# Optimization experiments

Hardware: AMD Instinct MI355X
Metric: run time of the kernel (lower is better)

The kernel has to match this reference:

```python
import jax, jax.numpy as jnp
import numpy as np
import math

B, S, E, H = 2, 2048, 2048, 16
HD = E // H // 2  # 64, per-head dim of each differential half
DEPTH = 12
LAMBDA_INIT = 0.8 - 0.6 * math.exp(-0.3 * DEPTH)
EPS = 1e-5


def setup_inputs() -> dict:
    key = jax.random.key(0)
    ks = jax.random.split(key, 10)
    sc = 0.02
    return {
        "x": jax.random.normal(ks[0], (B, S, E), jnp.float32),
        "Wq": jax.random.normal(ks[1], (E, E), jnp.float32) * sc,
        "Wk": jax.random.normal(ks[2], (E, E), jnp.float32) * sc,
        "Wv": jax.random.normal(ks[3], (E, E), jnp.float32) * sc,
        "Wo": jax.random.normal(ks[4], (E, E), jnp.float32) * sc,
        "lambda_q1": jax.random.normal(ks[5], (HD,), jnp.float32) * 0.1,
        "lambda_k1": jax.random.normal(ks[6], (HD,), jnp.float32) * 0.1,
        "lambda_q2": jax.random.normal(ks[7], (HD,), jnp.float32) * 0.1,
        "lambda_k2": jax.random.normal(ks[8], (HD,), jnp.float32) * 0.1,
        "gamma": jnp.ones((2 * HD,), jnp.float32),
    }


def _rope_interleaved(x, cos, sin):
    # x: [b, s, h, d]; cos/sin: [s, d//2]; pairs are (0,1),(2,3),...
    xe, xo = x[..., 0::2], x[..., 1::2]
    c = cos[None, :, None, :]
    s = sin[None, :, None, :]
    oe = xe * c - xo * s
    oo = xe * s + xo * c
    return jnp.stack([oe, oo], axis=-1).reshape(x.shape)


def reference(x, Wq, Wk, Wv, Wo, lambda_q1, lambda_k1, lambda_q2, lambda_k2, gamma):
    b, t, _ = x.shape
    # rotary tables (rotary dim == HD, interleaved)
    angle = 1.0 / 10000 ** jnp.linspace(0.0, 1.0, HD // 2, dtype=jnp.float32)
    freqs = jnp.arange(t, dtype=jnp.float32)[:, None] * angle  # [t, HD//2]
    cos, sin = jnp.cos(freqs), jnp.sin(freqs)

    q = (x @ Wq.T).reshape(b, t, 2 * H, HD)
    k = (x @ Wk.T).reshape(b, t, 2 * H, HD)
    v = (x @ Wv.T).reshape(b, t, H, 2 * HD)  # concat(v1, v2) along last dim

    q = _rope_interleaved(q, cos, sin)
    k = _rope_interleaved(k, cos, sin)

    q = q.reshape(b, t, H, 2, HD)
    k = k.reshape(b, t, H, 2, HD)
    q1, q2 = q[:, :, :, 0], q[:, :, :, 1]
    k1, k2 = k[:, :, :, 0], k[:, :, :, 1]

    scale = HD ** -0.5  # flash_attn default softmax scale
    # branch 1: softmax(q1 k1) @ [v1|v2]
    s1 = jnp.einsum("bthd,bshd->bhts", q1, k1) * scale
    p1 = jax.nn.softmax(s1, axis=-1)
    o1 = jnp.einsum("bhts,bshd->bthd", p1, v)  # [b,t,H,2*HD]
    # branch 2: softmax(q2 k2) @ [v1|v2]
    s2 = jnp.einsum("bthd,bshd->bhts", q2, k2) * scale
    p2 = jax.nn.softmax(s2, axis=-1)
    o2 = jnp.einsum("bhts,bshd->bthd", p2, v)

    lam1 = jnp.exp(jnp.sum(lambda_q1 * lambda_k1))
    lam2 = jnp.exp(jnp.sum(lambda_q2 * lambda_k2))
    lam = lam1 - lam2 + LAMBDA_INIT

    attn = o1 - lam * o2  # [b,t,H,2*HD]
    # RMSNorm over last dim (2*HD) with affine gamma
    rms = jax.lax.rsqrt(jnp.mean(attn * attn, axis=-1, keepdims=True) + EPS)
    attn = attn * rms * gamma
    attn = attn * (1.0 - LAMBDA_INIT)
    attn = attn.reshape(b, t, H * 2 * HD)
    return attn @ Wo.T
```

## Files before the change

kernel.cpp:

```cpp
#include <hip/hip_runtime.h>
#include <cstdint>
#include <cstddef>

typedef unsigned short u16;
typedef __attribute__((ext_vector_type(8))) short short8;
typedef __attribute__((ext_vector_type(4))) float f32x4;

#define MFMA_B16(a,b,c) __builtin_amdgcn_mfma_f32_16x16x32_bf16((a),(b),(c),0,0,0)

#define S_LEN 2048
#define EMB 2048
#define QKV_N 6144
#define HD 64
#define LAMBDA_INIT_F 0.78360576653162f
#define ONE_MINUS_LI 0.21639423346838f

static __device__ __forceinline__ u16 f2bf(float f) {
  unsigned u = __float_as_uint(f);
  unsigned r = ((u >> 16) & 1u) + 0x7fffu;
  return (u16)((u + r) >> 16);
}
static __device__ __forceinline__ float bf2f(u16 h) {
  return __uint_as_float(((unsigned)h) << 16);
}
static __device__ __forceinline__ unsigned cvt_pk_bf16(float lo, float hi) {
  unsigned r;
  asm("v_cvt_pk_bf16_f32 %0, %1, %2" : "=v"(r) : "v"(lo), "v"(hi));
  return r;
}
static __device__ __forceinline__ void gload_lds16(const u16* g, u16* l) {
  __builtin_amdgcn_global_load_lds((const __attribute__((address_space(1))) void*)g,
                                   (__attribute__((address_space(3))) void*)l, 16, 0, 0);
}

__global__ void cvt_f32_bf16(const float* __restrict__ s, u16* __restrict__ d, int n4) {
  int i = blockIdx.x * 256 + threadIdx.x;
  if (i >= n4) return;
  f32x4 v = *(const f32x4*)&s[i * 4];
  unsigned lo = cvt_pk_bf16(v[0], v[1]);
  unsigned hi = cvt_pk_bf16(v[2], v[3]);
  *(unsigned long long*)&d[i * 4] = (unsigned long long)lo | ((unsigned long long)hi << 32);
}

template <int BF16OUT>
__global__ __launch_bounds__(256, 2) void gemm_bt(const u16* __restrict__ A,
                                                  const u16* __restrict__ B,
                                                  void* __restrict__ Cout,
                                                  int M, int N, int K) {
  __shared__ u16 As[128 * 32];
  __shared__ u16 Bs[128 * 32];
  const int tid = threadIdx.x;
  const int lane = tid & 63, wv = tid >> 6;
  const int bm = blockIdx.x * 128, bn = blockIdx.y * 128;
  const int wr = (wv >> 1) * 64, wc = (wv & 1) * 64;
  const int lr = lane & 15, hk = lane >> 4;

  const int r0 = tid >> 2;
  const int c0 = (tid & 3) * 8;
  const u16* ga = A + (size_t)(bm + r0) * K + c0;
  const u16* gb = B + (size_t)(bn + r0) * K + c0;
  const size_t rstep = (size_t)64 * K;

  f32x4 acc[4][4] = {};

  for (int k0 = 0; k0 < K; k0 += 32) {
    __syncthreads();
    gload_lds16(ga + k0,         &As[(tid) * 8]);
    gload_lds16(ga + rstep + k0, &As[(tid + 256) * 8]);
    gload_lds16(gb + k0,         &Bs[(tid) * 8]);
    gload_lds16(gb + rstep + k0, &Bs[(tid + 256) * 8]);
    __syncthreads();
    short8 af[4], bfv[4];
#pragma unroll
    for (int i = 0; i < 4; i++) af[i] = *(const short8*)&As[(wr + i * 16 + lr) * 32 + hk * 8];
#pragma unroll
    for (int j = 0; j < 4; j++) bfv[j] = *(const short8*)&Bs[(wc + j * 16 + lr) * 32 + hk * 8];
#pragma unroll
    for (int i = 0; i < 4; i++)
#pragma unroll
      for (int j = 0; j < 4; j++)
        acc[i][j] = MFMA_B16(af[i], bfv[j], acc[i][j]);
  }

  if (BF16OUT) {
    u16* C = (u16*)Cout;
#pragma unroll
    for (int i = 0; i < 4; i++)
#pragma unroll
      for (int j = 0; j < 4; j++)
#pragma unroll
        for (int r = 0; r < 4; r++) {
          int row = bm + wr + i * 16 + hk * 4 + r;
          int col = bn + wc + j * 16 + lr;
          C[(size_t)row * N + col] = f2bf(acc[i][j][r]);
        }
  } else {
    float* C = (float*)Cout;
#pragma unroll
    for (int i = 0; i < 4; i++)
#pragma unroll
      for (int j = 0; j < 4; j++)
#pragma unroll
        for (int r = 0; r < 4; r++) {
          int row = bm + wr + i * 16 + hk * 4 + r;
          int col = bn + wc + j * 16 + lr;
          C[(size_t)row * N + col] = acc[i][j][r];
        }
  }
}

__global__ void rope_kernel(u16* __restrict__ qkv) {
  int idx = blockIdx.x * 256 + threadIdx.x;
  int p = idx & 31;
  int u = (idx >> 5) & 63;
  int m = idx >> 11;
  int t = m & (S_LEN - 1);
  int col = (u < 32) ? (u * 64 + 2 * p) : (EMB + (u - 32) * 64 + 2 * p);
  u16* ptr = qkv + (size_t)m * QKV_N + col;
  unsigned v = *(unsigned*)ptr;
  float xe = bf2f((u16)(v & 0xffff));
  float xo = bf2f((u16)(v >> 16));
  float w = expf((float)p * (-9.210340371976184f / 31.0f));
  float ang = (float)t * w;
  float sn, cs;
  sincosf(ang, &sn, &cs);
  float oe = xe * cs - xo * sn;
  float oo = xe * sn + xo * cs;
  *(unsigned*)ptr = (unsigned)f2bf(oe) | (((unsigned)f2bf(oo)) << 16);
}

#define SW(row, colByte) ((((row)) << 7) + ((colByte) ^ (((row) & 7) << 4)))

__global__ __launch_bounds__(256, 2) void attn_kernel(
    const u16* __restrict__ qkv, u16* __restrict__ attnb,
    const float* __restrict__ lq1, const float* __restrict__ lk1,
    const float* __restrict__ lq2, const float* __restrict__ lk2,
    const float* __restrict__ gamma) {
  __shared__ u16 K1s[64 * 64];
  __shared__ u16 K2s[64 * 64];
  __shared__ u16 VTs[128 * 64];
  __shared__ u16 Ps[4 * 2 * 16 * 64];

  const int g = blockIdx.x;
  const int xcd = g & 7;
  const int gi = g >> 3;
  const int bh = xcd * 4 + (gi >> 5);
  const int qt = gi & 31;
  const int b = bh >> 4, h = bh & 15;

  const int tid = threadIdx.x, lane = tid & 63, wv = tid >> 6;
  const int lr = lane & 15, hk = lane >> 4;

  float d1 = lq1[lane] * lk1[lane];
  float d2 = lq2[lane] * lk2[lane];
#pragma unroll
  for (int off = 32; off; off >>= 1) { d1 += __shfl_xor(d1, off); d2 += __shfl_xor(d2, off); }
  const float lam = __expf(d1) - __expf(d2) + LAMBDA_INIT_F;

  const int qrow = qt * 64 + wv * 16 + lr;
  const u16* qp = qkv + (size_t)(b * S_LEN + qrow) * QKV_N;
  short8 q1f[2], q2f[2];
  q1f[0] = *(const short8*)&qp[(2 * h) * 64 + hk * 8];
  q1f[1] = *(const short8*)&qp[(2 * h) * 64 + 32 + hk * 8];
  q2f[0] = *(const short8*)&qp[(2 * h + 1) * 64 + hk * 8];
  q2f[1] = *(const short8*)&qp[(2 * h + 1) * 64 + 32 + hk * 8];

  f32x4 o1a[8] = {};
  f32x4 o2a[8] = {};
  float l1p = 0.f, l2p = 0.f;

  const int gl_row = wv * 8 + (lane >> 3);
  const int gl_cb  = ((lane & 7) ^ (lane >> 3)) * 8;
  u16* k1d = &K1s[(wv * 8) * 64 + lane * 8];
  u16* k2d = &K2s[(wv * 8) * 64 + lane * 8];

  const int vkv = (tid & 31) * 2;
  const int vd0 = (tid >> 5) * 8;

  const u16* kb1 = qkv + (size_t)b * S_LEN * QKV_N + EMB + (2 * h) * 64;
  const u16* kb2 = kb1 + 64;
  const u16* vbp = qkv + (size_t)b * S_LEN * QKV_N + 2 * EMB + h * 128;

  char* P1 = (char*)&Ps[(wv * 2 + 0) * 16 * 64];
  char* P2 = (char*)&Ps[(wv * 2 + 1) * 16 * 64];
  char* VTc = (char*)VTs;

  for (int kv0 = 0; kv0 < S_LEN; kv0 += 64) {
    __syncthreads();
    {
      const u16* g1 = kb1 + (size_t)(kv0 + gl_row) * QKV_N + gl_cb;
      const u16* g2 = kb2 + (size_t)(kv0 + gl_row) * QKV_N + gl_cb;
      gload_lds16(g1, k1d);
      gload_lds16(g1 + (size_t)32 * QKV_N, k1d + 32 * 64);
      gload_lds16(g2, k2d);
      gload_lds16(g2 + (size_t)32 * QKV_N, k2d + 32 * 64);
    }
    {
      const u16* vs = vbp + (size_t)(kv0 + vkv) * QKV_N + vd0;
      short8 a0 = *(const short8*)vs;
      short8 a1 = *(const short8*)(vs + QKV_N);
      short8 b0 = *(const short8*)(vs + 64);
      short8 b1 = *(const short8*)(vs + QKV_N + 64);
#pragma unroll
      for (int j = 0; j < 8; j++) {
        unsigned pk0 = (unsigned)(u16)a0[j] | (((unsigned)(u16)a1[j]) << 16);
        *(unsigned*)(VTc + SW(vd0 + j, vkv * 2)) = pk0;
        unsigned pk1 = (unsigned)(u16)b0[j] | (((unsigned)(u16)b1[j]) << 16);
        *(unsigned*)(VTc + SW(vd0 + 64 + j, vkv * 2)) = pk1;
      }
    }
    __syncthreads();

#pragma unroll
    for (int st = 0; st < 2; st++) {
      const char* Ks = st ? (char*)K2s : (char*)K1s;
      const short8* qf = st ? q2f : q1f;
      char* Pw = st ? P2 : P1;
      float lacc = 0.f;
#pragma unroll
      for (int kt = 0; kt < 4; kt++) {
        f32x4 s = {0.f, 0.f, 0.f, 0.f};
        int row = kt * 16 + lr;
        short8 ka0 = *(const short8*)(Ks + SW(row, hk * 16));
        short8 ka1 = *(const short8*)(Ks + SW(row, 64 + hk * 16));
        s = MFMA_B16(ka0, qf[0], s);
        s = MFMA_B16(ka1, qf[1], s);
        float e0 = __expf(s[0] * 0.125f);
        float e1 = __expf(s[1] * 0.125f);
        float e2 = __expf(s[2] * 0.125f);
        float e3 = __expf(s[3] * 0.125f);
        lacc += (e0 + e1) + (e2 + e3);
        unsigned plo = cvt_pk_bf16(e0, e1);
        unsigned phi = cvt_pk_bf16(e2, e3);
        *(unsigned long long*)(Pw + SW(lr, kt * 32 + hk * 8)) =
            (unsigned long long)plo | ((unsigned long long)phi << 32);
      }
      if (st) l2p += lacc; else l1p += lacc;
    }
    asm volatile("" ::: "memory");

    short8 p10 = *(const short8*)(P1 + SW(lr, hk * 16));
    short8 p11 = *(const short8*)(P1 + SW(lr, 64 + hk * 16));
    short8 p20 = *(const short8*)(P2 + SW(lr, hk * 16));
    short8 p21 = *(const short8*)(P2 + SW(lr, 64 + hk * 16));
#pragma unroll
    for (int dt = 0; dt < 8; dt++) {
      int row = dt * 16 + lr;
      short8 va0 = *(const short8*)(VTc + SW(row, hk * 16));
      short8 va1 = *(const short8*)(VTc + SW(row, 64 + hk * 16));
      o1a[dt] = MFMA_B16(va0, p10, o1a[dt]);
      o1a[dt] = MFMA_B16(va1, p11, o1a[dt]);
      o2a[dt] = MFMA_B16(va0, p20, o2a[dt]);
      o2a[dt] = MFMA_B16(va1, p21, o2a[dt]);
    }
  }

  float l1 = l1p; l1 += __shfl_xor(l1, 16); l1 += __shfl_xor(l1, 32);
  float l2 = l2p; l2 += __shfl_xor(l2, 16); l2 += __shfl_xor(l2, 32);
  const float inv1 = 1.f / l1;
  const float inv2 = 1.f / l2;

  float av[8][4];
  float ss = 0.f;
#pragma unroll
  for (int dt = 0; dt < 8; dt++)
#pragma unroll
    for (int r = 0; r < 4; r++) {
      float a = o1a[dt][r] * inv1 - lam * (o2a[dt][r] * inv2);
      av[dt][r] = a;
      ss += a * a;
    }
  ss += __shfl_xor(ss, 16); ss += __shfl_xor(ss, 32);
  const float sc2 = rsqrtf(ss * (1.f / 128.f) + 1e-5f) * ONE_MINUS_LI;

  u16* orow = attnb + (size_t)(b * S_LEN + qrow) * EMB + h * 128;
#pragma unroll
  for (int dt = 0; dt < 8; dt++) {
    int d = dt * 16 + hk * 4;
    f32x4 gv = *(const f32x4*)&gamma[d];
    unsigned plo = cvt_pk_bf16(av[dt][0] * gv[0] * sc2, av[dt][1] * gv[1] * sc2);
    unsigned phi = cvt_pk_bf16(av[dt][2] * gv[2] * sc2, av[dt][3] * gv[3] * sc2);
    *(unsigned long long*)&orow[d] = (unsigned long long)plo | ((unsigned long long)phi << 32);
  }
}

extern "C" void kernel_launch(void* const* d_in, const int* in_sizes, int n_in,
                              void* d_out, int out_size, void* d_ws, size_t ws_size,
                              hipStream_t stream) {
  (void)in_sizes; (void)n_in; (void)out_size; (void)ws_size;
  const float* x   = (const float*)d_in[0];
  const float* Wq  = (const float*)d_in[1];
  const float* Wk  = (const float*)d_in[2];
  const float* Wv  = (const float*)d_in[3];
  const float* Wo  = (const float*)d_in[4];
  const float* lq1 = (const float*)d_in[5];
  const float* lk1 = (const float*)d_in[6];
  const float* lq2 = (const float*)d_in[7];
  const float* lk2 = (const float*)d_in[8];
  const float* gam = (const float*)d_in[9];

  char* ws = (char*)d_ws;
  u16* xb    = (u16*)(ws);
  u16* Wcat  = (u16*)(ws + 16777216);
  u16* Wob   = (u16*)(ws + 41943040);
  u16* qkv   = (u16*)(ws + 50331648);
  u16* attnb = xb;

  const int NE = EMB * EMB;
  cvt_f32_bf16<<<(2 * NE / 4 + 255) / 256, 256, 0, stream>>>(x, xb, 2 * NE / 4);
  cvt_f32_bf16<<<(NE / 4 + 255) / 256, 256, 0, stream>>>(Wq, Wcat, NE / 4);
  cvt_f32_bf16<<<(NE / 4 + 255) / 256, 256, 0, stream>>>(Wk, Wcat + NE, NE / 4);
  cvt_f32_bf16<<<(NE / 4 + 255) / 256, 256, 0, stream>>>(Wv, Wcat + 2 * NE, NE / 4);
  cvt_f32_bf16<<<(NE / 4 + 255) / 256, 256, 0, stream>>>(Wo, Wob, NE / 4);

  dim3 g1(4096 / 128, QKV_N / 128);
  gemm_bt<1><<<g1, 256, 0, stream>>>(xb, Wcat, qkv, 4096, QKV_N, EMB);

  rope_kernel<<<(4096 * 64 * 32) / 256, 256, 0, stream>>>(qkv);

  attn_kernel<<<1024, 256, 0, stream>>>(qkv, attnb, lq1, lk1, lq2, lk2, gam);

  dim3 g2(4096 / 128, EMB / 128);
  gemm_bt<0><<<g2, 256, 0, stream>>>(attnb, Wob, d_out, 4096, EMB, EMB);
}
```

Measured before the change: 360.9 us.

## Process two 16-row query tiles per wave to reuse K/V LDS loads

```diff
diff --git a/kernel.cpp b/kernel.cpp
--- a/kernel.cpp
+++ b/kernel.cpp
@@ -14,6 +14,7 @@
 #define HD 64
 #define LAMBDA_INIT_F 0.78360576653162f
 #define ONE_MINUS_LI 0.21639423346838f
+#define EXP2_SCALE 0.18033688011112042f
 
 static __device__ __forceinline__ u16 f2bf(float f) {
   unsigned u = __float_as_uint(f);
@@ -139,13 +140,13 @@
   __shared__ u16 K1s[64 * 64];
   __shared__ u16 K2s[64 * 64];
   __shared__ u16 VTs[128 * 64];
-  __shared__ u16 Ps[4 * 2 * 16 * 64];
+  __shared__ u16 Ps[4 * 4 * 16 * 64];
 
   const int g = blockIdx.x;
   const int xcd = g & 7;
   const int gi = g >> 3;
-  const int bh = xcd * 4 + (gi >> 5);
-  const int qt = gi & 31;
+  const int bh = xcd * 4 + (gi >> 4);
+  const int qt = gi & 15;
   const int b = bh >> 4, h = bh & 15;
 
   const int tid = threadIdx.x, lane = tid & 63, wv = tid >> 6;
@@ -157,17 +158,21 @@
   for (int off = 32; off; off >>= 1) { d1 += __shfl_xor(d1, off); d2 += __shfl_xor(d2, off); }
   const float lam = __expf(d1) - __expf(d2) + LAMBDA_INIT_F;
 
-  const int qrow = qt * 64 + wv * 16 + lr;
-  const u16* qp = qkv + (size_t)(b * S_LEN + qrow) * QKV_N;
-  short8 q1f[2], q2f[2];
-  q1f[0] = *(const short8*)&qp[(2 * h) * 64 + hk * 8];
-  q1f[1] = *(const short8*)&qp[(2 * h) * 64 + 32 + hk * 8];
-  q2f[0] = *(const short8*)&qp[(2 * h + 1) * 64 + hk * 8];
-  q2f[1] = *(const short8*)&qp[(2 * h + 1) * 64 + 32 + hk * 8];
-
-  f32x4 o1a[8] = {};
-  f32x4 o2a[8] = {};
-  float l1p = 0.f, l2p = 0.f;
+  const int qrowA = qt * 128 + wv * 32 + lr;
+  const int qrowB = qrowA + 16;
+  const u16* qpA = qkv + (size_t)(b * S_LEN + qrowA) * QKV_N;
+  const u16* qpB = qkv + (size_t)(b * S_LEN + qrowB) * QKV_N;
+  short8 q1fA0 = *(const short8*)&qpA[(2 * h) * 64 + hk * 8];
+  short8 q1fA1 = *(const short8*)&qpA[(2 * h) * 64 + 32 + hk * 8];
+  short8 q2fA0 = *(const short8*)&qpA[(2 * h + 1) * 64 + hk * 8];
+  short8 q2fA1 = *(const short8*)&qpA[(2 * h + 1) * 64 + 32 + hk * 8];
+  short8 q1fB0 = *(const short8*)&qpB[(2 * h) * 64 + hk * 8];
+  short8 q1fB1 = *(const short8*)&qpB[(2 * h) * 64 + 32 + hk * 8];
+  short8 q2fB0 = *(const short8*)&qpB[(2 * h + 1) * 64 + hk * 8];
+  short8 q2fB1 = *(const short8*)&qpB[(2 * h + 1) * 64 + 32 + hk * 8];
+
+  f32x4 o1A[8] = {}, o1B[8] = {}, o2A[8] = {}, o2B[8] = {};
+  float l1pA = 0.f, l1pB = 0.f, l2pA = 0.f, l2pB = 0.f;
 
   const int gl_row = wv * 8 + (lane >> 3);
   const int gl_cb  = ((lane & 7) ^ (lane >> 3)) * 8;
@@ -181,8 +186,10 @@
   const u16* kb2 = kb1 + 64;
   const u16* vbp = qkv + (size_t)b * S_LEN * QKV_N + 2 * EMB + h * 128;
 
-  char* P1 = (char*)&Ps[(wv * 2 + 0) * 16 * 64];
-  char* P2 = (char*)&Ps[(wv * 2 + 1) * 16 * 64];
+  char* P1A = (char*)&Ps[(wv * 4 + 0) * 16 * 64];
+  char* P1B = (char*)&Ps[(wv * 4 + 1) * 16 * 64];
+  char* P2A = (char*)&Ps[(wv * 4 + 2) * 16 * 64];
+  char* P2B = (char*)&Ps[(wv * 4 + 3) * 16 * 64];
   char* VTc = (char*)VTs;
 
   for (int kv0 = 0; kv0 < S_LEN; kv0 += 64) {
@@ -214,73 +221,121 @@
 #pragma unroll
     for (int st = 0; st < 2; st++) {
       const char* Ks = st ? (char*)K2s : (char*)K1s;
-      const short8* qf = st ? q2f : q1f;
-      char* Pw = st ? P2 : P1;
-      float lacc = 0.f;
+      const short8 qa0 = st ? q2fA0 : q1fA0;
+      const short8 qa1 = st ? q2fA1 : q1fA1;
+      const short8 qb0 = st ? q2fB0 : q1fB0;
+      const short8 qb1 = st ? q2fB1 : q1fB1;
+      char* PwA = st ? P2A : P1A;
+      char* PwB = st ? P2B : P1B;
+      float laccA = 0.f, laccB = 0.f;
 #pragma unroll
       for (int kt = 0; kt < 4; kt++) {
-        f32x4 s = {0.f, 0.f, 0.f, 0.f};
         int row = kt * 16 + lr;
         short8 ka0 = *(const short8*)(Ks + SW(row, hk * 16));
         short8 ka1 = *(const short8*)(Ks + SW(row, 64 + hk * 16));
-        s = MFMA_B16(ka0, qf[0], s);
-        s = MFMA_B16(ka1, qf[1], s);
-        float e0 = __expf(s[0] * 0.125f);
-        float e1 = __expf(s[1] * 0.125f);
-        float e2 = __expf(s[2] * 0.125f);
-        float e3 = __expf(s[3] * 0.125f);
-        lacc += (e0 + e1) + (e2 + e3);
-        unsigned plo = cvt_pk_bf16(e0, e1);
-        unsigned phi = cvt_pk_bf16(e2, e3);
-        *(unsigned long long*)(Pw + SW(lr, kt * 32 + hk * 8)) =
-            (unsigned long long)plo | ((unsigned long long)phi << 32);
+        f32x4 sA = {0.f, 0.f, 0.f, 0.f};
+        sA = MFMA_B16(ka0, qa0, sA);
+        sA = MFMA_B16(ka1, qa1, sA);
+        f32x4 sB = {0.f, 0.f, 0.f, 0.f};
+        sB = MFMA_B16(ka0, qb0, sB);
+        sB = MFMA_B16(ka1, qb1, sB);
+        float eA0 = __builtin_amdgcn_exp2f(sA[0] * EXP2_SCALE);
+        float eA1 = __builtin_amdgcn_exp2f(sA[1] * EXP2_SCALE);
+        float eA2 = __builtin_amdgcn_exp2f(sA[2] * EXP2_SCALE);
+        float eA3 = __builtin_amdgcn_exp2f(sA[3] * EXP2_SCALE);
+        laccA += (eA0 + eA1) + (eA2 + eA3);
+        unsigned pa0 = cvt_pk_bf16(eA0, eA1);
+        unsigned pa1 = cvt_pk_bf16(eA2, eA3);
+        *(unsigned long long*)(PwA + SW(lr, kt * 32 + hk * 8)) =
+            (unsigned long long)pa0 | ((unsigned long long)pa1 << 32);
+        float eB0 = __builtin_amdgcn_exp2f(sB[0] * EXP2_SCALE);
+        float eB1 = __builtin_amdgcn_exp2f(sB[1] * EXP2_SCALE);
+        float eB2 = __builtin_amdgcn_exp2f(sB[2] * EXP2_SCALE);
+        float eB3 = __builtin_amdgcn_exp2f(sB[3] * EXP2_SCALE);
+        laccB += (eB0 + eB1) + (eB2 + eB3);
+        unsigned pb0 = cvt_pk_bf16(eB0, eB1);
+        unsigned pb1 = cvt_pk_bf16(eB2, eB3);
+        *(unsigned long long*)(PwB + SW(lr, kt * 32 + hk * 8)) =
+            (unsigned long long)pb0 | ((unsigned long long)pb1 << 32);
       }
-      if (st) l2p += lacc; else l1p += lacc;
+      if (st) { l2pA += laccA; l2pB += laccB; }
+      else    { l1pA += laccA; l1pB += laccB; }
     }
     asm volatile("" ::: "memory");
 
-    short8 p10 = *(const short8*)(P1 + SW(lr, hk * 16));
-    short8 p11 = *(const short8*)(P1 + SW(lr, 64 + hk * 16));
-    short8 p20 = *(const short8*)(P2 + SW(lr, hk * 16));
-    short8 p21 = *(const short8*)(P2 + SW(lr, 64 + hk * 16));
+    short8 p10A = *(const short8*)(P1A + SW(lr, hk * 16));
+    short8 p11A = *(const short8*)(P1A + SW(lr, 64 + hk * 16));
+    short8 p10B = *(const short8*)(P1B + SW(lr, hk * 16));
+    short8 p11B = *(const short8*)(P1B + SW(lr, 64 + hk * 16));
+    short8 p20A = *(const short8*)(P2A + SW(lr, hk * 16));
+    short8 p21A = *(const short8*)(P2A + SW(lr, 64 + hk * 16));
+    short8 p20B = *(const short8*)(P2B + SW(lr, hk * 16));
+    short8 p21B = *(const short8*)(P2B + SW(lr, 64 + hk * 16));
 #pragma unroll
     for (int dt = 0; dt < 8; dt++) {
       int row = dt * 16 + lr;
       short8 va0 = *(const short8*)(VTc + SW(row, hk * 16));
       short8 va1 = *(const short8*)(VTc + SW(row, 64 + hk * 16));
-      o1a[dt] = MFMA_B16(va0, p10, o1a[dt]);
-      o1a[dt] = MFMA_B16(va1, p11, o1a[dt]);
-      o2a[dt] = MFMA_B16(va0, p20, o2a[dt]);
-      o2a[dt] = MFMA_B16(va1, p21, o2a[dt]);
-    }
-  }
-
-  float l1 = l1p; l1 += __shfl_xor(l1, 16); l1 += __shfl_xor(l1, 32);
-  float l2 = l2p; l2 += __shfl_xor(l2, 16); l2 += __shfl_xor(l2, 32);
-  const float inv1 = 1.f / l1;
-  const float inv2 = 1.f / l2;
-
-  float av[8][4];
-  float ss = 0.f;
-#pragma unroll
-  for (int dt = 0; dt < 8; dt++)
-#pragma unroll
-    for (int r = 0; r < 4; r++) {
-      float a = o1a[dt][r] * inv1 - lam * (o2a[dt][r] * inv2);
-      av[dt][r] = a;
-      ss += a * a;
-    }
-  ss += __shfl_xor(ss, 16); ss += __shfl_xor(ss, 32);
-  const float sc2 = rsqrtf(ss * (1.f / 128.f) + 1e-5f) * ONE_MINUS_LI;
-
-  u16* orow = attnb + (size_t)(b * S_LEN + qrow) * EMB + h * 128;
-#pragma unroll
-  for (int dt = 0; dt < 8; dt++) {
-    int d = dt * 16 + hk * 4;
-    f32x4 gv = *(const f32x4*)&gamma[d];
-    unsigned plo = cvt_pk_bf16(av[dt][0] * gv[0] * sc2, av[dt][1] * gv[1] * sc2);
-    unsigned phi = cvt_pk_bf16(av[dt][2] * gv[2] * sc2, av[dt][3] * gv[3] * sc2);
-    *(unsigned long long*)&orow[d] = (unsigned long long)plo | ((unsigned long long)phi << 32);
+      o1A[dt] = MFMA_B16(va0, p10A, o1A[dt]);
+      o1A[dt] = MFMA_B16(va1, p11A, o1A[dt]);
+      o1B[dt] = MFMA_B16(va0, p10B, o1B[dt]);
+      o1B[dt] = MFMA_B16(va1, p11B, o1B[dt]);
+      o2A[dt] = MFMA_B16(va0, p20A, o2A[dt]);
+      o2A[dt] = MFMA_B16(va1, p21A, o2A[dt]);
+      o2B[dt] = MFMA_B16(va0, p20B, o2B[dt]);
+      o2B[dt] = MFMA_B16(va1, p21B, o2B[dt]);
+    }
+  }
+
+  {
+    float l1 = l1pA; l1 += __shfl_xor(l1, 16); l1 += __shfl_xor(l1, 32);
+    float l2 = l2pA; l2 += __shfl_xor(l2, 16); l2 += __shfl_xor(l2, 32);
+    const float inv1 = 1.f / l1, inv2 = 1.f / l2;
+    float ss = 0.f;
+#pragma unroll
+    for (int dt = 0; dt < 8; dt++)
+#pragma unroll
+      for (int r = 0; r < 4; r++) {
+        float a = o1A[dt][r] * inv1 - lam * (o2A[dt][r] * inv2);
+        o1A[dt][r] = a;
+        ss += a * a;
+      }
+    ss += __shfl_xor(ss, 16); ss += __shfl_xor(ss, 32);
+    const float sc2 = rsqrtf(ss * (1.f / 128.f) + 1e-5f) * ONE_MINUS_LI;
+    u16* orow = attnb + (size_t)(b * S_LEN + qrowA) * EMB + h * 128;
+#pragma unroll
+    for (int dt = 0; dt < 8; dt++) {
+      int d = dt * 16 + hk * 4;
+      f32x4 gv = *(const f32x4*)&gamma[d];
+      unsigned plo = cvt_pk_bf16(o1A[dt][0] * gv[0] * sc2, o1A[dt][1] * gv[1] * sc2);
+      unsigned phi = cvt_pk_bf16(o1A[dt][2] * gv[2] * sc2, o1A[dt][3] * gv[3] * sc2);
+      *(unsigned long long*)&orow[d] = (unsigned long long)plo | ((unsigned long long)phi << 32);
+    }
+  }
+  {
+    float l1 = l1pB; l1 += __shfl_xor(l1, 16); l1 += __shfl_xor(l1, 32);
+    float l2 = l2pB; l2 += __shfl_xor(l2, 16); l2 += __shfl_xor(l2, 32);
+    const float inv1 = 1.f / l1, inv2 = 1.f / l2;
+    float ss = 0.f;
+#pragma unroll
+    for (int dt = 0; dt < 8; dt++)
+#pragma unroll
+      for (int r = 0; r < 4; r++) {
+        float a = o1B[dt][r] * inv1 - lam * (o2B[dt][r] * inv2);
+        o1B[dt][r] = a;
+        ss += a * a;
+      }
+    ss += __shfl_xor(ss, 16); ss += __shfl_xor(ss, 32);
+    const float sc2 = rsqrtf(ss * (1.f / 128.f) + 1e-5f) * ONE_MINUS_LI;
+    u16* orow = attnb + (size_t)(b * S_LEN + qrowB) * EMB + h * 128;
+#pragma unroll
+    for (int dt = 0; dt < 8; dt++) {
+      int d = dt * 16 + hk * 4;
+      f32x4 gv = *(const f32x4*)&gamma[d];
+      unsigned plo = cvt_pk_bf16(o1B[dt][0] * gv[0] * sc2, o1B[dt][1] * gv[1] * sc2);
+      unsigned phi = cvt_pk_bf16(o1B[dt][2] * gv[2] * sc2, o1B[dt][3] * gv[3] * sc2);
+      *(unsigned long long*)&orow[d] = (unsigned long long)plo | ((unsigned long long)phi << 32);
+    }
   }
 }
 
@@ -318,7 +373,7 @@
 
   rope_kernel<<<(4096 * 64 * 32) / 256, 256, 0, stream>>>(qkv);
 
-  attn_kernel<<<1024, 256, 0, stream>>>(qkv, attnb, lq1, lk1, lq2, lk2, gam);
+  attn_kernel<<<512, 256, 0, stream>>>(qkv, attnb, lq1, lk1, lq2, lk2, gam);
 
   dim3 g2(4096 / 128, EMB / 128);
   gemm_bt<0><<<g2, 256, 0, stream>>>(attnb, Wob, d_out, 4096, EMB, EMB);
```

After: 401.8 us. +11.3%, slower.

## Switch attention to 32x32x16 MFMA with 128-row query tiles per block

Applied to the files above, without the earlier changes.

```diff
diff --git a/kernel.cpp b/kernel.cpp
--- a/kernel.cpp
+++ b/kernel.cpp
@@ -5,8 +5,10 @@
 typedef unsigned short u16;
 typedef __attribute__((ext_vector_type(8))) short short8;
 typedef __attribute__((ext_vector_type(4))) float f32x4;
+typedef __attribute__((ext_vector_type(16))) float f32x16;
 
 #define MFMA_B16(a,b,c) __builtin_amdgcn_mfma_f32_16x16x32_bf16((a),(b),(c),0,0,0)
+#define MFMA32(a,b,c)  __builtin_amdgcn_mfma_f32_32x32x16_bf16((a),(b),(c),0,0,0)
 
 #define S_LEN 2048
 #define EMB 2048
@@ -14,6 +16,7 @@
 #define HD 64
 #define LAMBDA_INIT_F 0.78360576653162f
 #define ONE_MINUS_LI 0.21639423346838f
+#define EXP2_SCALE 0.18033688011112042f
 
 static __device__ __forceinline__ u16 f2bf(float f) {
   unsigned u = __float_as_uint(f);
@@ -131,6 +134,38 @@
 
 #define SW(row, colByte) ((((row)) << 7) + ((colByte) ^ (((row) & 7) << 4)))
 
+#define QKT(Kc, Q0, Q1, Q2, Q3, KT, Pc, LSUM)                                    \
+  do {                                                                           \
+    f32x16 s = {};                                                               \
+    s = MFMA32(*(const short8*)((Kc) + SW((KT) * 32 + l31, 0  + hi16)), Q0, s);  \
+    s = MFMA32(*(const short8*)((Kc) + SW((KT) * 32 + l31, 32 + hi16)), Q1, s);  \
+    s = MFMA32(*(const short8*)((Kc) + SW((KT) * 32 + l31, 64 + hi16)), Q2, s);  \
+    s = MFMA32(*(const short8*)((Kc) + SW((KT) * 32 + l31, 96 + hi16)), Q3, s);  \
+    _Pragma("unroll") for (int r = 0; r < 16; r += 4) {                          \
+      float e0 = __builtin_amdgcn_exp2f(s[r]     * EXP2_SCALE);                  \
+      float e1 = __builtin_amdgcn_exp2f(s[r + 1] * EXP2_SCALE);                  \
+      float e2 = __builtin_amdgcn_exp2f(s[r + 2] * EXP2_SCALE);                  \
+      float e3 = __builtin_amdgcn_exp2f(s[r + 3] * EXP2_SCALE);                  \
+      LSUM += (e0 + e1) + (e2 + e3);                                             \
+      unsigned lo_ = cvt_pk_bf16(e0, e1);                                        \
+      unsigned hi_ = cvt_pk_bf16(e2, e3);                                        \
+      *(unsigned long long*)((Pc) + SW(l31, (KT) * 64 + (r >> 2) * 16 + hi8)) =  \
+          (unsigned long long)lo_ | ((unsigned long long)hi_ << 32);             \
+    }                                                                            \
+  } while (0)
+
+#define PVD(DT, O1, O2)                                                          \
+  do {                                                                           \
+    short8 va0 = *(const short8*)(VTc + SW((DT) * 32 + l31, 0  + hi16));         \
+    short8 va1 = *(const short8*)(VTc + SW((DT) * 32 + l31, 32 + hi16));         \
+    short8 va2 = *(const short8*)(VTc + SW((DT) * 32 + l31, 64 + hi16));         \
+    short8 va3 = *(const short8*)(VTc + SW((DT) * 32 + l31, 96 + hi16));         \
+    O1 = MFMA32(va0, p1f0, O1); O1 = MFMA32(va1, p1f1, O1);                      \
+    O1 = MFMA32(va2, p1f2, O1); O1 = MFMA32(va3, p1f3, O1);                      \
+    O2 = MFMA32(va0, p2f0, O2); O2 = MFMA32(va1, p2f1, O2);                      \
+    O2 = MFMA32(va2, p2f2, O2); O2 = MFMA32(va3, p2f3, O2);                      \
+  } while (0)
+
 __global__ __launch_bounds__(256, 2) void attn_kernel(
     const u16* __restrict__ qkv, u16* __restrict__ attnb,
     const float* __restrict__ lq1, const float* __restrict__ lk1,
@@ -139,17 +174,20 @@
   __shared__ u16 K1s[64 * 64];
   __shared__ u16 K2s[64 * 64];
   __shared__ u16 VTs[128 * 64];
-  __shared__ u16 Ps[4 * 2 * 16 * 64];
+  __shared__ u16 Ps[4 * 2 * 32 * 64];
 
   const int g = blockIdx.x;
   const int xcd = g & 7;
   const int gi = g >> 3;
-  const int bh = xcd * 4 + (gi >> 5);
-  const int qt = gi & 31;
+  const int bh = xcd * 4 + (gi >> 4);
+  const int qt = gi & 15;
   const int b = bh >> 4, h = bh & 15;
 
   const int tid = threadIdx.x, lane = tid & 63, wv = tid >> 6;
-  const int lr = lane & 15, hk = lane >> 4;
+  const int l31 = lane & 31;
+  const int hi16 = (lane >> 5) * 16;
+  const int hi8 = (lane >> 5) * 8;
+  const int hi4 = (lane >> 5) * 4;
 
   float d1 = lq1[lane] * lk1[lane];
   float d2 = lq2[lane] * lk2[lane];
@@ -157,16 +195,20 @@
   for (int off = 32; off; off >>= 1) { d1 += __shfl_xor(d1, off); d2 += __shfl_xor(d2, off); }
   const float lam = __expf(d1) - __expf(d2) + LAMBDA_INIT_F;
 
-  const int qrow = qt * 64 + wv * 16 + lr;
-  const u16* qp = qkv + (size_t)(b * S_LEN + qrow) * QKV_N;
-  short8 q1f[2], q2f[2];
-  q1f[0] = *(const short8*)&qp[(2 * h) * 64 + hk * 8];
-  q1f[1] = *(const short8*)&qp[(2 * h) * 64 + 32 + hk * 8];
-  q2f[0] = *(const short8*)&qp[(2 * h + 1) * 64 + hk * 8];
-  q2f[1] = *(const short8*)&qp[(2 * h + 1) * 64 + 32 + hk * 8];
-
-  f32x4 o1a[8] = {};
-  f32x4 o2a[8] = {};
+  const int qbase = qt * 128 + wv * 32;
+  const u16* qp1 = qkv + (size_t)(b * S_LEN + qbase + l31) * QKV_N + (2 * h) * 64;
+  const u16* qp2 = qp1 + 64;
+  short8 q1f0 = *(const short8*)(qp1 + hi8);
+  short8 q1f1 = *(const short8*)(qp1 + 16 + hi8);
+  short8 q1f2 = *(const short8*)(qp1 + 32 + hi8);
+  short8 q1f3 = *(const short8*)(qp1 + 48 + hi8);
+  short8 q2f0 = *(const short8*)(qp2 + hi8);
+  short8 q2f1 = *(const short8*)(qp2 + 16 + hi8);
+  short8 q2f2 = *(const short8*)(qp2 + 32 + hi8);
+  short8 q2f3 = *(const short8*)(qp2 + 48 + hi8);
+
+  f32x16 o1t0 = {}, o1t1 = {}, o1t2 = {}, o1t3 = {};
+  f32x16 o2t0 = {}, o2t1 = {}, o2t2 = {}, o2t3 = {};
   float l1p = 0.f, l2p = 0.f;
 
   const int gl_row = wv * 8 + (lane >> 3);
@@ -181,9 +223,11 @@
   const u16* kb2 = kb1 + 64;
   const u16* vbp = qkv + (size_t)b * S_LEN * QKV_N + 2 * EMB + h * 128;
 
-  char* P1 = (char*)&Ps[(wv * 2 + 0) * 16 * 64];
-  char* P2 = (char*)&Ps[(wv * 2 + 1) * 16 * 64];
+  char* K1c = (char*)K1s;
+  char* K2c = (char*)K2s;
   char* VTc = (char*)VTs;
+  char* P1c = (char*)&Ps[(wv * 2 + 0) * 32 * 64];
+  char* P2c = (char*)&Ps[(wv * 2 + 1) * 32 * 64];
 
   for (int kv0 = 0; kv0 < S_LEN; kv0 += 64) {
     __syncthreads();
@@ -211,77 +255,56 @@
     }
     __syncthreads();
 
-#pragma unroll
-    for (int st = 0; st < 2; st++) {
-      const char* Ks = st ? (char*)K2s : (char*)K1s;
-      const short8* qf = st ? q2f : q1f;
-      char* Pw = st ? P2 : P1;
-      float lacc = 0.f;
-#pragma unroll
-      for (int kt = 0; kt < 4; kt++) {
-        f32x4 s = {0.f, 0.f, 0.f, 0.f};
-        int row = kt * 16 + lr;
-        short8 ka0 = *(const short8*)(Ks + SW(row, hk * 16));
-        short8 ka1 = *(const short8*)(Ks + SW(row, 64 + hk * 16));
-        s = MFMA_B16(ka0, qf[0], s);
-        s = MFMA_B16(ka1, qf[1], s);
-        float e0 = __expf(s[0] * 0.125f);
-        float e1 = __expf(s[1] * 0.125f);
-        float e2 = __expf(s[2] * 0.125f);
-        float e3 = __expf(s[3] * 0.125f);
-        lacc += (e0 + e1) + (e2 + e3);
-        unsigned plo = cvt_pk_bf16(e0, e1);
-        unsigned phi = cvt_pk_bf16(e2, e3);
-        *(unsigned long long*)(Pw + SW(lr, kt * 32 + hk * 8)) =
-            (unsigned long long)plo | ((unsigned long long)phi << 32);
-      }
-      if (st) l2p += lacc; else l1p += lacc;
-    }
+    QKT(K1c, q1f0, q1f1, q1f2, q1f3, 0, P1c, l1p);
+    QKT(K1c, q1f0, q1f1, q1f2, q1f3, 1, P1c, l1p);
+    QKT(K2c, q2f0, q2f1, q2f2, q2f3, 0, P2c, l2p);
+    QKT(K2c, q2f0, q2f1, q2f2, q2f3, 1, P2c, l2p);
     asm volatile("" ::: "memory");
 
-    short8 p10 = *(const short8*)(P1 + SW(lr, hk * 16));
-    short8 p11 = *(const short8*)(P1 + SW(lr, 64 + hk * 16));
-    short8 p20 = *(const short8*)(P2 + SW(lr, hk * 16));
-    short8 p21 = *(const short8*)(P2 + SW(lr, 64 + hk * 16));
-#pragma unroll
-    for (int dt = 0; dt < 8; dt++) {
-      int row = dt * 16 + lr;
-      short8 va0 = *(const short8*)(VTc + SW(row, hk * 16));
-      short8 va1 = *(const short8*)(VTc + SW(row, 64 + hk * 16));
-      o1a[dt] = MFMA_B16(va0, p10, o1a[dt]);
-      o1a[dt] = MFMA_B16(va1, p11, o1a[dt]);
-      o2a[dt] = MFMA_B16(va0, p20, o2a[dt]);
-      o2a[dt] = MFMA_B16(va1, p21, o2a[dt]);
-    }
-  }
-
-  float l1 = l1p; l1 += __shfl_xor(l1, 16); l1 += __shfl_xor(l1, 32);
-  float l2 = l2p; l2 += __shfl_xor(l2, 16); l2 += __shfl_xor(l2, 32);
+    short8 p1f0 = *(const short8*)(P1c + SW(l31, 0  + hi16));
+    short8 p1f1 = *(const short8*)(P1c + SW(l31, 32 + hi16));
+    short8 p1f2 = *(const short8*)(P1c + SW(l31, 64 + hi16));
+    short8 p1f3 = *(const short8*)(P1c + SW(l31, 96 + hi16));
+    short8 p2f0 = *(const short8*)(P2c + SW(l31, 0  + hi16));
+    short8 p2f1 = *(const short8*)(P2c + SW(l31, 32 + hi16));
+    short8 p2f2 = *(const short8*)(P2c + SW(l31, 64 + hi16));
+    short8 p2f3 = *(const short8*)(P2c + SW(l31, 96 + hi16));
+
+    PVD(0, o1t0, o2t0);
+    PVD(1, o1t1, o2t1);
+    PVD(2, o1t2, o2t2);
+    PVD(3, o1t3, o2t3);
+    asm volatile("" ::: "memory");
+  }
+
+  float l1 = l1p + __shfl_xor(l1p, 32);
+  float l2 = l2p + __shfl_xor(l2p, 32);
   const float inv1 = 1.f / l1;
   const float inv2 = 1.f / l2;
 
-  float av[8][4];
   float ss = 0.f;
-#pragma unroll
-  for (int dt = 0; dt < 8; dt++)
-#pragma unroll
-    for (int r = 0; r < 4; r++) {
-      float a = o1a[dt][r] * inv1 - lam * (o2a[dt][r] * inv2);
-      av[dt][r] = a;
-      ss += a * a;
-    }
-  ss += __shfl_xor(ss, 16); ss += __shfl_xor(ss, 32);
+#define COMB(O1, O2)                                                   \
+  _Pragma("unroll") for (int i = 0; i < 16; i++) {                     \
+    float a = O1[i] * inv1 - lam * (O2[i] * inv2);                     \
+    O1[i] = a;                                                         \
+    ss += a * a;                                                       \
+  }
+  COMB(o1t0, o2t0) COMB(o1t1, o2t1) COMB(o1t2, o2t2) COMB(o1t3, o2t3)
+#undef COMB
+  ss += __shfl_xor(ss, 32);
   const float sc2 = rsqrtf(ss * (1.f / 128.f) + 1e-5f) * ONE_MINUS_LI;
 
-  u16* orow = attnb + (size_t)(b * S_LEN + qrow) * EMB + h * 128;
-#pragma unroll
-  for (int dt = 0; dt < 8; dt++) {
-    int d = dt * 16 + hk * 4;
-    f32x4 gv = *(const f32x4*)&gamma[d];
-    unsigned plo = cvt_pk_bf16(av[dt][0] * gv[0] * sc2, av[dt][1] * gv[1] * sc2);
-    unsigned phi = cvt_pk_bf16(av[dt][2] * gv[2] * sc2, av[dt][3] * gv[3] * sc2);
-    *(unsigned long long*)&orow[d] = (unsigned long long)plo | ((unsigned long long)phi << 32);
-  }
+  u16* orow = attnb + (size_t)(b * S_LEN + qbase + l31) * EMB + h * 128;
+#define WRT(O1, T)                                                              \
+  _Pragma("unroll") for (int gg = 0; gg < 4; gg++) {                            \
+    int d = (T) * 32 + gg * 8 + hi4;                                            \
+    f32x4 gv = *(const f32x4*)&gamma[d];                                        \
+    unsigned wlo = cvt_pk_bf16(O1[4 * gg] * gv[0] * sc2, O1[4 * gg + 1] * gv[1] * sc2); \
+    unsigned whi = cvt_pk_bf16(O1[4 * gg + 2] * gv[2] * sc2, O1[4 * gg + 3] * gv[3] * sc2); \
+    *(unsigned long long*)&orow[d] = (unsigned long long)wlo | ((unsigned long long)whi << 32); \
+  }
+  WRT(o1t0, 0) WRT(o1t1, 1) WRT(o1t2, 2) WRT(o1t3, 3)
+#undef WRT
 }
 
 extern "C" void kernel_launch(void* const* d_in, const int* in_sizes, int n_in,
@@ -318,7 +341,7 @@
 
   rope_kernel<<<(4096 * 64 * 32) / 256, 256, 0, stream>>>(qkv);
 
-  attn_kernel<<<1024, 256, 0, stream>>>(qkv, attnb, lq1, lk1, lq2, lk2, gam);
+  attn_kernel<<<512, 256, 0, stream>>>(qkv, attnb, lq1, lk1, lq2, lk2, gam);
 
   dim3 g2(4096 / 128, EMB / 128);
   gemm_bt<0><<<g2, 256, 0, stream>>>(attnb, Wob, d_out, 4096, EMB, EMB);
```

Result: slower. 375.2 us (+4.0%).
